# Optimization experiments

Measured on AMD Instinct MI355X. Metric: run time of the kernel, lower is better.

The kernel has to match this reference:

```python
import jax, jax.numpy as jnp
import numpy as np

N_NODES = 100000
N_EDGES = 1600000
F_IN = 64
F_HID = 64
CURV = 1.0          # fixed curvature for every layer (args.c)
MIN_NORM = 1e-15    # HGCN min_norm clamp
PROJ_EPS = 4e-3     # HGCN float32 boundary eps


def _artanh(x):
    x = jnp.clip(x, -1.0 + 1e-7, 1.0 - 1e-7)
    return 0.5 * (jnp.log1p(x) - jnp.log1p(-x))


def _norm(x):
    return jnp.sqrt(jnp.clip(jnp.sum(x * x, axis=-1, keepdims=True), MIN_NORM))


def proj(x, c):
    # clip points to the open Poincare ball of radius (1-eps)/sqrt(c)
    maxnorm = (1.0 - PROJ_EPS) / jnp.sqrt(c)
    n = _norm(x)
    return jnp.where(n > maxnorm, x / n * maxnorm, x)


def expmap0(u, c):
    sc = jnp.sqrt(c)
    n = _norm(u)
    return jnp.tanh(sc * n) * u / (sc * n)


def logmap0(p, c):
    sc = jnp.sqrt(c)
    n = _norm(p)
    return _artanh(sc * n) * p / (sc * n)


def mobius_add(x, y, c):
    x2 = jnp.sum(x * x, -1, keepdims=True)
    y2 = jnp.sum(y * y, -1, keepdims=True)
    xy = jnp.sum(x * y, -1, keepdims=True)
    num = (1.0 + 2.0 * c * xy + c * y2) * x + (1.0 - c * x2) * y
    den = 1.0 + 2.0 * c * xy + c * c * x2 * y2
    return num / jnp.clip(den, MIN_NORM)


def mobius_matvec(M, x, c):
    sc = jnp.sqrt(c)
    xn = _norm(x)
    mx = x @ M.T                       # [N, out]
    mxn = _norm(mx)
    res = jnp.tanh(mxn / xn * _artanh(sc * xn)) * mx / (mxn * sc)
    zero = jnp.all(mx == 0, axis=-1, keepdims=True)
    return jnp.where(zero, jnp.zeros_like(res), res)


def hyp_linear(x, W, b, c):
    res = proj(mobius_matvec(W, x, c), c)
    hyp_b = proj(expmap0(b.reshape(1, -1), c), c)   # proj_tan0 is identity on Poincare ball
    return proj(mobius_add(res, hyp_b, c), c)


def hyp_agg(x, src, dst, w, c, n_nodes):
    xt = logmap0(x, c)                              # tangent space at origin
    msg = xt[src] * w[:, None]                      # [E, d] gather + weight
    agg = jax.ops.segment_sum(msg, dst, num_segments=n_nodes)  # spmm(adj, xt)
    return proj(expmap0(agg, c), c)


def hyp_act(x, c_in, c_out):
    xt = jax.nn.relu(logmap0(x, c_in))              # act in tangent space
    return proj(expmap0(xt, c_out), c_out)          # proj_tan0 identity


def hgnn_layer(x, W, b, src, dst, w, c_in, c_out, n_nodes):
    h = hyp_linear(x, W, b, c_in)
    h = hyp_agg(h, src, dst, w, c_in, n_nodes)
    return hyp_act(h, c_in, c_out)


def setup_inputs() -> dict:
    key = jax.random.key(0)
    ks = jax.random.split(key, 7)
    x = jax.random.normal(ks[0], (N_NODES, F_IN), dtype=jnp.float32)
    edge_index = jax.random.randint(ks[1], (2, N_EDGES), 0, N_NODES, dtype=jnp.int64 if jax.config.jax_enable_x64 else jnp.int32)
    edge_weight = jax.random.uniform(ks[2], (N_EDGES,), dtype=jnp.float32) / 16.0
    W0 = jax.random.normal(ks[3], (F_HID, F_IN), dtype=jnp.float32) * 0.1
    b0 = jax.random.normal(ks[4], (F_HID,), dtype=jnp.float32) * 0.1
    W1 = jax.random.normal(ks[5], (F_HID, F_HID), dtype=jnp.float32) * 0.1
    b1 = jax.random.normal(ks[6], (F_HID,), dtype=jnp.float32) * 0.1
    return {"x": x, "edge_index": edge_index, "edge_weight": edge_weight,
            "W0": W0, "b0": b0, "W1": W1, "b1": b1}


def reference(x, edge_index, edge_weight, W0, b0, W1, b1):
    src, dst = edge_index[0], edge_index[1]
    # encode(): proj_tan0 (identity for Poincare ball) -> expmap0 -> proj
    h = proj(expmap0(x, CURV), CURV)
    h = hgnn_layer(h, W0, b0, src, dst, edge_weight, CURV, CURV, N_NODES)
    h = hgnn_layer(h, W1, b1, src, dst, edge_weight, CURV, CURV, N_NODES)
    return h
```

## Files before the change

### kernel.cpp

```cpp
#include <hip/hip_runtime.h>
#include <hip/hip_bf16.h>
#include <stdint.h>

#define MIN_NORM 1e-15f
#define MAXNORM 0.996f
#define ART_CLIP 0.9999999f
#define CAP 5120
#define BKT_NODES 256
#define W_SCALE 524288.f
#define W_INV   (1.f / 524288.f)
#define CUR_STRIDE 16

typedef __attribute__((ext_vector_type(8))) short s8v;
typedef __attribute__((ext_vector_type(4))) float f4v;
typedef __attribute__((ext_vector_type(4))) unsigned u4v;

__device__ __forceinline__ float rcp_f(float x) { return __builtin_amdgcn_rcpf(x); }

__device__ __forceinline__ float fast_tanh(float x) {
    float e = __expf(2.f * x);
    return 1.f - 2.f * rcp_f(e + 1.f);
}
__device__ __forceinline__ float fast_artanh(float x) {
    x = fminf(x, ART_CLIP);
    return 0.5f * __logf((1.f + x) * rcp_f(1.f - x));
}

__device__ __forceinline__ float wsum(float v) {
#pragma unroll
    for (int m = 32; m >= 1; m >>= 1) v += __shfl_xor(v, m, 64);
    return v;
}
__device__ __forceinline__ unsigned wave_iscan(unsigned v, int lane) {
#pragma unroll
    for (int d = 1; d < 64; d <<= 1) {
        unsigned o = __shfl_up(v, d, 64);
        if (lane >= d) v += o;
    }
    return v;
}

__device__ __forceinline__ unsigned short f2bf(float f) {
    unsigned u = __builtin_bit_cast(unsigned, f);
    u += 0x7FFFu + ((u >> 16) & 1u);
    return (unsigned short)(u >> 16);
}
__device__ __forceinline__ float bf2f(unsigned short h) {
    return __builtin_bit_cast(float, (unsigned)h << 16);
}
__device__ __forceinline__ float bfu_lo(unsigned v) {
    return __builtin_bit_cast(float, v << 16);
}
__device__ __forceinline__ float bfu_hi(unsigned v) {
    return __builtin_bit_cast(float, v & 0xFFFF0000u);
}

__global__ void __launch_bounds__(1024) k_part(const int* __restrict__ dst,
                                               const int* __restrict__ src,
                                               const float* __restrict__ ew,
                                               unsigned* __restrict__ bktCur,
                                               int2* __restrict__ part, int E, int NB) {
    __shared__ unsigned lcnt[512], lbase[512];
    const int tid = threadIdx.x;
    const int BT = blockDim.x;
    const int PB = gridDim.x;
    const int chunk = (E + PB - 1) / PB;
    const int lo = blockIdx.x * chunk, hi = min(lo + chunk, E);
    for (int i = tid; i < NB; i += BT) lcnt[i] = 0;
    __syncthreads();
    for (int e = lo + tid; e < hi; e += BT)
        atomicAdd(&lcnt[(unsigned)dst[e] >> 8], 1u);
    __syncthreads();
    for (int i = tid; i < NB; i += BT) {
        unsigned c = lcnt[i];
        lbase[i] = c ? atomicAdd(&bktCur[i * CUR_STRIDE], c) : 0u;
        lcnt[i] = 0;
    }
    __syncthreads();
    for (int e = lo + tid; e < hi; e += BT) {
        int d = dst[e];
        int bkt = (unsigned)d >> 8;
        unsigned r = atomicAdd(&lcnt[bkt], 1u);
        unsigned rel = lbase[bkt] + r;
        if (rel < CAP)
            part[(size_t)bkt * CAP + rel] =
                make_int2(((d & 255) << 17) | src[e], __float_as_int(ew[e]));
    }
}

__device__ __forceinline__ void sort_body(const int2* __restrict__ part,
                                          const unsigned* __restrict__ bktCur,
                                          unsigned* __restrict__ part2,
                                          int2* __restrict__ off2, int nNodes, int b) {
    const int base = b * CAP;
    const int cnt = min((int)bktCur[b * CUR_STRIDE], CAP);
    const int tid = threadIdx.x, lane = tid & 63, wid = tid >> 6;
    __shared__ unsigned hist[256];
    __shared__ unsigned wpart[4];
    hist[tid] = 0;
    __syncthreads();
    for (int i = tid; i < cnt; i += 256)
        atomicAdd(&hist[(unsigned)part[base + i].x >> 17], 1u);
    __syncthreads();
    unsigned h = hist[tid];
    unsigned inc = wave_iscan(h, lane);
    if (lane == 63) wpart[wid] = inc;
    __syncthreads();
    unsigned wo = 0;
    for (int i = 0; i < wid; ++i) wo += wpart[i];
    unsigned start = wo + inc - h;
    int node = b * BKT_NODES + tid;
    if (node < nNodes)
        off2[node] = make_int2(base + (int)start, base + (int)(start + h));
    __syncthreads();
    hist[tid] = start;
    __syncthreads();
    for (int i = tid; i < cnt; i += 256) {
        int2 m = part[base + i];
        unsigned r = atomicAdd(&hist[(unsigned)m.x >> 17], 1u);
        float w = __int_as_float(m.y);
        unsigned fw = (unsigned)__float2uint_rn(w * W_SCALE);
        if (fw > 32767u) fw = 32767u;
        part2[base + r] = (fw << 17) | ((unsigned)m.x & 0x1FFFFu);
    }
}

template <bool ENCODE>
__device__ __forceinline__ void lin_scalars(float n2, float m2, float d, float y2,
                                            float& lam, float& mu) {
    float nx = sqrtf(fmaxf(n2, MIN_NORM));
    float xn = ENCODE ? fminf(fast_tanh(nx), MAXNORM) : nx;
    float sm = sqrtf(fmaxf(m2, MIN_NORM));
    float ratio = sm * rcp_f(nx);
    float tt = fminf(fast_tanh(ratio * fast_artanh(xn)), MAXNORM);
    float rho = tt * rcp_f(sm);
    float xy = rho * d;
    float x2 = tt * tt;
    float den = fmaxf(1.f + 2.f * xy + x2 * y2, MIN_NORM);
    float iden = rcp_f(den);
    float A = (1.f + 2.f * xy + y2) * iden;
    float B = (1.f - x2) * iden;
    float on2 = A * A * x2 + 2.f * A * B * xy + B * B * y2;
    float on = sqrtf(fmaxf(on2, MIN_NORM));
    float g = on > MAXNORM ? MAXNORM * rcp_f(on) : 1.f;
    float onc = fminf(on, MAXNORM);
    float L = fast_artanh(onc) * rcp_f(onc) * g;
    lam = L * A * rho;
    mu  = L * B;
}

struct LinCtx {
    s8v wfh[4][2], wfl[4][2];
    float hbr[4][4];
    float y2;
};
template <typename CTX>
__device__ __forceinline__ void lin_prologue(const float* __restrict__ W,
                                             const float* __restrict__ braw,
                                             float* shb, CTX& c, int col, int q) {
    const int tid = threadIdx.x;
    if (tid < 64) {
        float u = braw[tid];
        float n = sqrtf(fmaxf(wsum(u * u), MIN_NORM));
        float t = tanhf(n);
        float h = t * u / n;
        float hn = sqrtf(fmaxf(wsum(h * h), MIN_NORM));
        if (hn > MAXNORM) h *= MAXNORM / hn;
        shb[tid] = h;
        float y2 = wsum(h * h);
        if (tid == 0) shb[64] = y2;
    }
    __syncthreads();
#pragma unroll
    for (int f = 0; f < 4; ++f) {
#pragma unroll
        for (int s = 0; s < 2; ++s) {
            const float4 a4 = *(const float4*)(W + (size_t)(16 * f + col) * 64 + 4 * q + 32 * s);
            const float4 b4 = *(const float4*)(W + (size_t)(16 * f + col) * 64 + 4 * q + 16 + 32 * s);
            float v[8] = {a4.x, a4.y, a4.z, a4.w, b4.x, b4.y, b4.z, b4.w};
            s8v h8, l8;
#pragma unroll
            for (int e = 0; e < 8; ++e) {
                unsigned short hb_ = f2bf(v[e]);
                float hf = bf2f(hb_);
                h8[e] = (short)hb_;
                l8[e] = (short)f2bf(v[e] - hf);
            }
            c.wfh[f][s] = h8;
            c.wfl[f][s] = l8;
        }
#pragma unroll
        for (int r = 0; r < 4; ++r) c.hbr[f][r] = shb[16 * f + 4 * q + r];
    }
    c.y2 = shb[64];
}

template <bool ENCODE>
__device__ __forceinline__ void lin_epilogue(const LinCtx& c, f4v* acc, float n2p,
                                             unsigned short* __restrict__ xt_out,
                                             int node, bool ok, int q) {
    float m2p = 0.f, dp = 0.f;
#pragma unroll
    for (int f = 0; f < 4; ++f)
#pragma unroll
        for (int r = 0; r < 4; ++r) {
            float mv = acc[f][r];
            m2p = fmaf(mv, mv, m2p);
            dp  = fmaf(mv, c.hbr[f][r], dp);
        }
#pragma unroll
    for (int m = 16; m <= 32; m <<= 1) {
        n2p += __shfl_xor(n2p, m, 64);
        m2p += __shfl_xor(m2p, m, 64);
        dp  += __shfl_xor(dp,  m, 64);
    }
    float lam, mu;
    lin_scalars<ENCODE>(n2p, m2p, dp, c.y2, lam, mu);
    if (ok) {
#pragma unroll
        for (int f = 0; f < 4; ++f) {
            float r0 = fmaf(lam, acc[f][0], mu * c.hbr[f][0]);
            float r1 = fmaf(lam, acc[f][1], mu * c.hbr[f][1]);
            float r2 = fmaf(lam, acc[f][2], mu * c.hbr[f][2]);
            float r3 = fmaf(lam, acc[f][3], mu * c.hbr[f][3]);
            uint2 pk;
            pk.x = (unsigned)f2bf(r0) | ((unsigned)f2bf(r1) << 16);
            pk.y = (unsigned)f2bf(r2) | ((unsigned)f2bf(r3) << 16);
            *(uint2*)(xt_out + (size_t)node * 64 + 16 * f + 4 * q) = pk;
        }
    }
}

__device__ __forceinline__ void lin_body_f32(const float* __restrict__ xin,
                                             const float* __restrict__ W,
                                             const float* __restrict__ braw,
                                             unsigned short* __restrict__ xt_out,
                                             int nNodes, int nTiles, int blk, int LB) {
    __shared__ float shb[65];
    const int tid = threadIdx.x;
    const int lane = tid & 63, wid = tid >> 6;
    const int col = lane & 15, q = lane >> 4;
    LinCtx c;
    lin_prologue(W, braw, shb, c, col, q);

    const int nw = LB * 4;
    for (int t = blk * 4 + wid; t < nTiles; t += nw) {
        const int node = t * 16 + col;
        const bool ok = node < nNodes;
        const int ldn = ok ? node : (nNodes - 1);
        float n2p = 0.f;
        s8v xh[2], xl[2];
#pragma unroll
        for (int s = 0; s < 2; ++s) {
            const float4 a4 = *(const float4*)(xin + (size_t)ldn * 64 + 4 * q + 32 * s);
            const float4 b4 = *(const float4*)(xin + (size_t)ldn * 64 + 4 * q + 16 + 32 * s);
            float xv[8] = {a4.x, a4.y, a4.z, a4.w, b4.x, b4.y, b4.z, b4.w};
            s8v h8, l8;
#pragma unroll
            for (int e = 0; e < 8; ++e) {
                float xe = xv[e];
                n2p = fmaf(xe, xe, n2p);
                unsigned short hb_ = f2bf(xe);
                float hf = bf2f(hb_);
                h8[e] = (short)hb_;
                l8[e] = (short)f2bf(xe - hf);
            }
            xh[s] = h8;
            xl[s] = l8;
        }
        f4v acc[4];
#pragma unroll
        for (int f = 0; f < 4; ++f) acc[f] = (f4v){0.f, 0.f, 0.f, 0.f};
#pragma unroll
        for (int s = 0; s < 2; ++s) {
#pragma unroll
            for (int f = 0; f < 4; ++f)
                acc[f] = __builtin_amdgcn_mfma_f32_16x16x32_bf16(c.wfh[f][s], xh[s], acc[f], 0, 0, 0);
#pragma unroll
            for (int f = 0; f < 4; ++f)
                acc[f] = __builtin_amdgcn_mfma_f32_16x16x32_bf16(c.wfh[f][s], xl[s], acc[f], 0, 0, 0);
#pragma unroll
            for (int f = 0; f < 4; ++f)
                acc[f] = __builtin_amdgcn_mfma_f32_16x16x32_bf16(c.wfl[f][s], xh[s], acc[f], 0, 0, 0);
        }
        lin_epilogue<true>(c, acc, n2p, xt_out, node, ok, q);
    }
}

__global__ void __launch_bounds__(256, 2) k_mid(const int2* __restrict__ part,
                                                const unsigned* __restrict__ bktCur,
                                                unsigned* __restrict__ part2,
                                                int2* __restrict__ off2, int NB,
                                                const float* __restrict__ x,
                                                const float* __restrict__ W0,
                                                const float* __restrict__ b0,
                                                unsigned short* __restrict__ xt,
                                                int nNodes, int nTiles, int LB) {
    if ((int)blockIdx.x < NB)
        sort_body(part, bktCur, part2, off2, nNodes, blockIdx.x);
    else
        lin_body_f32(x, W0, b0, xt, nNodes, nTiles, blockIdx.x - NB, LB);
}

__global__ void __launch_bounds__(256, 2) k_linb(const unsigned short* __restrict__ xin,
                                                 const float* __restrict__ W,
                                                 const float* __restrict__ braw,
                                                 unsigned short* __restrict__ xt_out,
                                                 int nNodes, int nTiles) {
    __shared__ float shb[65];
    const int tid = threadIdx.x;
    const int lane = tid & 63, wid = tid >> 6;
    const int col = lane & 15, q = lane >> 4;
    LinCtx c;
    lin_prologue(W, braw, shb, c, col, q);

    const int nw = gridDim.x * 4;
    for (int t = blockIdx.x * 4 + wid; t < nTiles; t += nw) {
        const int node = t * 16 + col;
        const bool ok = node < nNodes;
        const int ldn = ok ? node : (nNodes - 1);
        const unsigned short* rp = xin + (size_t)ldn * 64;
        uint2 A = *(const uint2*)(rp + 4 * q);
        uint2 B = *(const uint2*)(rp + 4 * q + 16);
        uint2 C = *(const uint2*)(rp + 4 * q + 32);
        uint2 D = *(const uint2*)(rp + 4 * q + 48);
        u4v t0 = {A.x, A.y, B.x, B.y};
        u4v t1 = {C.x, C.y, D.x, D.y};
        s8v xh0 = __builtin_bit_cast(s8v, t0);
        s8v xh1 = __builtin_bit_cast(s8v, t1);
        float n2p = 0.f;
        {
            unsigned uu[8] = {A.x, A.y, B.x, B.y, C.x, C.y, D.x, D.y};
#pragma unroll
            for (int e = 0; e < 8; ++e) {
                float lo = bfu_lo(uu[e]), hi = bfu_hi(uu[e]);
                n2p = fmaf(lo, lo, n2p);
                n2p = fmaf(hi, hi, n2p);
            }
        }
        f4v acc[4];
#pragma unroll
        for (int f = 0; f < 4; ++f) acc[f] = (f4v){0.f, 0.f, 0.f, 0.f};
#pragma unroll
        for (int f = 0; f < 4; ++f)
            acc[f] = __builtin_amdgcn_mfma_f32_16x16x32_bf16(c.wfh[f][0], xh0, acc[f], 0, 0, 0);
#pragma unroll
        for (int f = 0; f < 4; ++f)
            acc[f] = __builtin_amdgcn_mfma_f32_16x16x32_bf16(c.wfl[f][0], xh0, acc[f], 0, 0, 0);
#pragma unroll
        for (int f = 0; f < 4; ++f)
            acc[f] = __builtin_amdgcn_mfma_f32_16x16x32_bf16(c.wfh[f][1], xh1, acc[f], 0, 0, 0);
#pragma unroll
        for (int f = 0; f < 4; ++f)
            acc[f] = __builtin_amdgcn_mfma_f32_16x16x32_bf16(c.wfl[f][1], xh1, acc[f], 0, 0, 0);
        lin_epilogue<false>(c, acc, n2p, xt_out, node, ok, q);
    }
}

template <bool BF16OUT>
__global__ void __launch_bounds__(256) k_agg(const unsigned short* __restrict__ xt,
                                             const unsigned* __restrict__ meta,
                                             const int2* __restrict__ off2,
                                             void* __restrict__ hout, int nNodes) {
    const int tid = threadIdx.x;
    const int lane = tid & 63;
    const int h = lane >> 5;
    const int j = lane & 31;
    const int hbase = h << 5;
    const int nw = gridDim.x * (blockDim.x >> 6);
    const int nPairs = (nNodes + 1) >> 1;
    int pair = blockIdx.x * (blockDim.x >> 6) + (tid >> 6);
    if (pair >= nPairs) return;
    int node = pair * 2 + h;
    int2 rng = (node < nNodes) ? off2[node] : make_int2(0, 0);
    while (true) {
        const int nxt = pair + nw;
        int2 rngN = make_int2(0, 0);
        if (nxt < nPairs) {
            int nn = nxt * 2 + h;
            if (nn < nNodes) rngN = off2[nn];
        }
        const bool okn = node < nNodes;
        const int s0 = rng.x;
        const int deg = rng.y - rng.x;
        unsigned mp = 0;
        if (j < deg) mp = meta[s0 + j];
        const int kmax = min(deg, 32);
        const int kOther = __shfl(kmax, lane ^ 32, 64);
        const int kCeil = (max(kmax, kOther) + 7) & ~7;
        float a0 = 0.f, a1 = 0.f, b0_ = 0.f, b1_ = 0.f;
        for (int k = 0; k < kCeil; k += 8) {
            unsigned p0 = __shfl(mp, hbase + k, 64);
            unsigned p1 = __shfl(mp, hbase + k + 1, 64);
            unsigned p2 = __shfl(mp, hbase + k + 2, 64);
            unsigned p3 = __shfl(mp, hbase + k + 3, 64);
            unsigned p4 = __shfl(mp, hbase + k + 4, 64);
            unsigned p5 = __shfl(mp, hbase + k + 5, 64);
            unsigned p6 = __shfl(mp, hbase + k + 6, 64);
            unsigned p7 = __shfl(mp, hbase + k + 7, 64);
            unsigned v0 = *(const unsigned*)(xt + (((p0 & 0x1FFFFu) << 6) + 2 * j));
            unsigned v1 = *(const unsigned*)(xt + (((p1 & 0x1FFFFu) << 6) + 2 * j));
            unsigned v2 = *(const unsigned*)(xt + (((p2 & 0x1FFFFu) << 6) + 2 * j));
            unsigned v3 = *(const unsigned*)(xt + (((p3 & 0x1FFFFu) << 6) + 2 * j));
            unsigned v4 = *(const unsigned*)(xt + (((p4 & 0x1FFFFu) << 6) + 2 * j));
            unsigned v5 = *(const unsigned*)(xt + (((p5 & 0x1FFFFu) << 6) + 2 * j));
            unsigned v6 = *(const unsigned*)(xt + (((p6 & 0x1FFFFu) << 6) + 2 * j));
            unsigned v7 = *(const unsigned*)(xt + (((p7 & 0x1FFFFu) << 6) + 2 * j));
            float w0 = (float)(p0 >> 17);
            float w1 = (float)(p1 >> 17);
            float w2 = (float)(p2 >> 17);
            float w3 = (float)(p3 >> 17);
            float w4 = (float)(p4 >> 17);
            float w5 = (float)(p5 >> 17);
            float w6 = (float)(p6 >> 17);
            float w7 = (float)(p7 >> 17);
            a0 = fmaf(bfu_lo(v0), w0, a0);   a1 = fmaf(bfu_hi(v0), w0, a1);
            b0_ = fmaf(bfu_lo(v1), w1, b0_); b1_ = fmaf(bfu_hi(v1), w1, b1_);
            a0 = fmaf(bfu_lo(v2), w2, a0);   a1 = fmaf(bfu_hi(v2), w2, a1);
            b0_ = fmaf(bfu_lo(v3), w3, b0_); b1_ = fmaf(bfu_hi(v3), w3, b1_);
            a0 = fmaf(bfu_lo(v4), w4, a0);   a1 = fmaf(bfu_hi(v4), w4, a1);
            b0_ = fmaf(bfu_lo(v5), w5, b0_); b1_ = fmaf(bfu_hi(v5), w5, b1_);
            a0 = fmaf(bfu_lo(v6), w6, a0);   a1 = fmaf(bfu_hi(v6), w6, a1);
            b0_ = fmaf(bfu_lo(v7), w7, b0_); b1_ = fmaf(bfu_hi(v7), w7, b1_);
        }
        for (int kk = s0 + 32; kk < rng.y; ++kk) {
            unsigned pv = meta[kk];
            unsigned v = *(const unsigned*)(xt + (((pv & 0x1FFFFu) << 6) + 2 * j));
            float wv2 = (float)(pv >> 17);
            a0 = fmaf(bfu_lo(v), wv2, a0);
            a1 = fmaf(bfu_hi(v), wv2, a1);
        }
        float acc0 = (a0 + b0_) * W_INV, acc1 = (a1 + b1_) * W_INV;
        float r0 = fmaxf(acc0, 0.f), r1 = fmaxf(acc1, 0.f);
        float sA = fmaf(acc0, acc0, acc1 * acc1);
        float sR = fmaf(r0, r0, r1 * r1);
#pragma unroll
        for (int mm = 1; mm <= 16; mm <<= 1) {
            sA += __shfl_xor(sA, mm, 64);
            sR += __shfl_xor(sR, mm, 64);
        }
        float n = sqrtf(fmaxf(sA, MIN_NORM));
        float t = fast_tanh(n);
        float g1 = t > MAXNORM ? MAXNORM * rcp_f(t) : 1.f;
        float tc = fminf(t, MAXNORM);
        float alpha = fast_artanh(tc) * rcp_f(tc) * g1 * t * rcp_f(n);
        float mnorm = sqrtf(fmaxf(alpha * alpha * sR, MIN_NORM));
        float t2 = fast_tanh(mnorm);
        float g2 = t2 > MAXNORM ? MAXNORM * rcp_f(t2) : 1.f;
        float gamma = t2 * rcp_f(mnorm) * g2 * alpha;
        if (okn) {
            if (BF16OUT) {
                unsigned pk = (unsigned)f2bf(gamma * r0) |
                              ((unsigned)f2bf(gamma * r1) << 16);
                ((unsigned*)hout)[(size_t)node * 32 + j] = pk;
            } else {
                float2 o;
                o.x = gamma * r0;
                o.y = gamma * r1;
                *(float2*)((float*)hout + (size_t)node * 64 + 2 * j) = o;
            }
        }
        if (nxt >= nPairs) break;
        pair = nxt;
        node = pair * 2 + h;
        rng = rngN;
    }
}

extern "C" void kernel_launch(void* const* d_in, const int* in_sizes, int n_in,
                              void* d_out, int out_size, void* d_ws, size_t ws_size,
                              hipStream_t stream) {
    const float* x   = (const float*)d_in[0];
    const int*   ei  = (const int*)d_in[1];
    const float* ew  = (const float*)d_in[2];
    const float* W0  = (const float*)d_in[3];
    const float* b0  = (const float*)d_in[4];
    const float* W1  = (const float*)d_in[5];
    const float* b1  = (const float*)d_in[6];
    const int N = in_sizes[0] / 64;
    const int E = in_sizes[2];
    const int* src = ei;
    const int* dst = ei + E;
    const int NB = (N + BKT_NODES - 1) / BKT_NODES;
    const int nTiles = (N + 15) / 16;
    const int LB = 1024;

    uint8_t* p = (uint8_t*)d_ws;
    auto carve = [&](size_t bytes) { uint8_t* q = p; p += (bytes + 255) & ~(size_t)255; return q; };
    unsigned*       bktCur = (unsigned*)carve((size_t)NB * CUR_STRIDE * 4);
    int2*           part   = (int2*)carve((size_t)NB * CAP * 8);
    unsigned*       part2  = (unsigned*)carve((size_t)NB * CAP * 4);
    int2*           off2   = (int2*)carve((size_t)N * 8);
    unsigned short* xt     = (unsigned short*)carve((size_t)N * 64 * 2);
    unsigned short* hb16   = (unsigned short*)carve((size_t)N * 64 * 2);

    hipMemsetAsync(bktCur, 0, (size_t)NB * CUR_STRIDE * 4, stream);
    k_part<<<256, 1024, 0, stream>>>(dst, src, ew, bktCur, part, E, NB);
    k_mid<<<NB + LB, 256, 0, stream>>>(part, bktCur, part2, off2, NB,
                                       x, W0, b0, xt, N, nTiles, LB);
    k_agg<true><<<4096, 256, 0, stream>>>(xt, part2, off2, hb16, N);
    k_linb<<<1024, 256, 0, stream>>>(hb16, W1, b1, xt, N, nTiles);
    k_agg<false><<<4096, 256, 0, stream>>>(xt, part2, off2, d_out, N);
}
```

Before: 146.7 us.

## Co-schedule edge partitioning with first hyperbolic linear layer, split out sort kernel

Moves the first-layer linear transform out of the sort kernel and into the partition kernel's launch, using 512-thread blocks. The partition blocks and linear blocks now run concurrently, and bucket sorting becomes its own kernel. The aim is to overlap the memory-bound edge partitioning with the MFMA linear work instead of overlapping sort with linear. The trade-off is that partitioning now runs with 512 threads per block instead of 1024, and the linear work is spread across fewer, larger blocks.

```diff
diff --git a/kernel.cpp b/kernel.cpp
--- a/kernel.cpp
+++ b/kernel.cpp
@@ -55,17 +55,16 @@
     return __builtin_bit_cast(float, v & 0xFFFF0000u);
 }
 
-__global__ void __launch_bounds__(1024) k_part(const int* __restrict__ dst,
-                                               const int* __restrict__ src,
-                                               const float* __restrict__ ew,
-                                               unsigned* __restrict__ bktCur,
-                                               int2* __restrict__ part, int E, int NB) {
-    __shared__ unsigned lcnt[512], lbase[512];
+__device__ __forceinline__ void part_body(const int* __restrict__ dst,
+                                          const int* __restrict__ src,
+                                          const float* __restrict__ ew,
+                                          unsigned* __restrict__ bktCur,
+                                          int2* __restrict__ part, int E, int NB,
+                                          int blk, int PB, unsigned* lcnt, unsigned* lbase) {
     const int tid = threadIdx.x;
     const int BT = blockDim.x;
-    const int PB = gridDim.x;
     const int chunk = (E + PB - 1) / PB;
-    const int lo = blockIdx.x * chunk, hi = min(lo + chunk, E);
+    const int lo = blk * chunk, hi = min(lo + chunk, E);
     for (int i = tid; i < NB; i += BT) lcnt[i] = 0;
     __syncthreads();
     for (int e = lo + tid; e < hi; e += BT)
@@ -88,10 +87,11 @@
     }
 }
 
-__device__ __forceinline__ void sort_body(const int2* __restrict__ part,
-                                          const unsigned* __restrict__ bktCur,
-                                          unsigned* __restrict__ part2,
-                                          int2* __restrict__ off2, int nNodes, int b) {
+__global__ void __launch_bounds__(256) k_sort(const int2* __restrict__ part,
+                                              const unsigned* __restrict__ bktCur,
+                                              unsigned* __restrict__ part2,
+                                              int2* __restrict__ off2, int nNodes) {
+    const int b = blockIdx.x;
     const int base = b * CAP;
     const int cnt = min((int)bktCur[b * CUR_STRIDE], CAP);
     const int tid = threadIdx.x, lane = tid & 63, wid = tid >> 6;
@@ -154,10 +154,9 @@
     float hbr[4][4];
     float y2;
 };
-template <typename CTX>
 __device__ __forceinline__ void lin_prologue(const float* __restrict__ W,
                                              const float* __restrict__ braw,
-                                             float* shb, CTX& c, int col, int q) {
+                                             float* shb, LinCtx& c, int col, int q) {
     const int tid = threadIdx.x;
     if (tid < 64) {
         float u = braw[tid];
@@ -235,16 +234,17 @@
                                              const float* __restrict__ W,
                                              const float* __restrict__ braw,
                                              unsigned short* __restrict__ xt_out,
-                                             int nNodes, int nTiles, int blk, int LB) {
-    __shared__ float shb[65];
+                                             int nNodes, int nTiles, int blk, int LB,
+                                             float* shb) {
     const int tid = threadIdx.x;
     const int lane = tid & 63, wid = tid >> 6;
     const int col = lane & 15, q = lane >> 4;
+    const int WPB = blockDim.x >> 6;
     LinCtx c;
     lin_prologue(W, braw, shb, c, col, q);
 
-    const int nw = LB * 4;
-    for (int t = blk * 4 + wid; t < nTiles; t += nw) {
+    const int nw = LB * WPB;
+    for (int t = blk * WPB + wid; t < nTiles; t += nw) {
         const int node = t * 16 + col;
         const bool ok = node < nNodes;
         const int ldn = ok ? node : (nNodes - 1);
@@ -287,19 +287,21 @@
     }
 }
 
-__global__ void __launch_bounds__(256, 2) k_mid(const int2* __restrict__ part,
-                                                const unsigned* __restrict__ bktCur,
-                                                unsigned* __restrict__ part2,
-                                                int2* __restrict__ off2, int NB,
-                                                const float* __restrict__ x,
-                                                const float* __restrict__ W0,
-                                                const float* __restrict__ b0,
-                                                unsigned short* __restrict__ xt,
-                                                int nNodes, int nTiles, int LB) {
-    if ((int)blockIdx.x < NB)
-        sort_body(part, bktCur, part2, off2, nNodes, blockIdx.x);
+__global__ void __launch_bounds__(512) k_pre(const int* __restrict__ dst,
+                                             const int* __restrict__ src,
+                                             const float* __restrict__ ew,
+                                             unsigned* __restrict__ bktCur,
+                                             int2* __restrict__ part, int E, int NB,
+                                             const float* __restrict__ x,
+                                             const float* __restrict__ W0,
+                                             const float* __restrict__ b0,
+                                             unsigned short* __restrict__ xt,
+                                             int nNodes, int nTiles, int PB, int LB) {
+    __shared__ unsigned sh[1024];
+    if ((int)blockIdx.x < PB)
+        part_body(dst, src, ew, bktCur, part, E, NB, blockIdx.x, PB, sh, sh + 512);
     else
-        lin_body_f32(x, W0, b0, xt, nNodes, nTiles, blockIdx.x - NB, LB);
+        lin_body_f32(x, W0, b0, xt, nNodes, nTiles, blockIdx.x - PB, LB, (float*)sh);
 }
 
 __global__ void __launch_bounds__(256, 2) k_linb(const unsigned short* __restrict__ xin,
@@ -483,7 +485,7 @@
     const int* dst = ei + E;
     const int NB = (N + BKT_NODES - 1) / BKT_NODES;
     const int nTiles = (N + 15) / 16;
-    const int LB = 1024;
+    const int PB = 256, LB = 512;
 
     uint8_t* p = (uint8_t*)d_ws;
     auto carve = [&](size_t bytes) { uint8_t* q = p; p += (bytes + 255) & ~(size_t)255; return q; };
@@ -495,9 +497,9 @@
     unsigned short* hb16   = (unsigned short*)carve((size_t)N * 64 * 2);
 
     hipMemsetAsync(bktCur, 0, (size_t)NB * CUR_STRIDE * 4, stream);
-    k_part<<<256, 1024, 0, stream>>>(dst, src, ew, bktCur, part, E, NB);
-    k_mid<<<NB + LB, 256, 0, stream>>>(part, bktCur, part2, off2, NB,
-                                       x, W0, b0, xt, N, nTiles, LB);
+    k_pre<<<PB + LB, 512, 0, stream>>>(dst, src, ew, bktCur, part, E, NB,
+                                       x, W0, b0, xt, N, nTiles, PB, LB);
+    k_sort<<<NB, 256, 0, stream>>>(part, bktCur, part2, off2, N);
     k_agg<true><<<4096, 256, 0, stream>>>(xt, part2, off2, hb16, N);
     k_linb<<<1024, 256, 0, stream>>>(hb16, W1, b1, xt, N, nTiles);
     k_agg<false><<<4096, 256, 0, stream>>>(xt, part2, off2, d_out, N);
```

After: 150.8 us. 2.8% more time.
